# Optimization experiments

Measured on AMD Instinct MI355X. Metric: run time of the kernel, lower is better.

The kernel has to match this reference:

```python
import jax, jax.numpy as jnp
import numpy as np

B, L, IN, HID, D3 = 32, 8192, 512, 512, 128

def setup_inputs() -> dict:
    key = jax.random.key(0)
    ks = jax.random.split(key, 7)
    s_in = 1.0 / np.sqrt(IN)
    s_h = 1.0 / np.sqrt(HID)
    return {
        'inputs': jax.random.normal(ks[0], (B, IN), jnp.float32),
        'context': jax.random.normal(ks[1], (B, L, HID), jnp.float32),
        'Wi': jax.random.uniform(ks[2], (D3, IN), jnp.float32, -s_in, s_in),
        'bi': jax.random.uniform(ks[3], (D3,), jnp.float32, -s_in, s_in),
        'Wh': jax.random.uniform(ks[4], (D3, HID), jnp.float32, -s_h, s_h),
        'bh': jax.random.uniform(ks[5], (D3,), jnp.float32, -s_h, s_h),
        'V': jax.random.uniform(ks[6], (D3,), jnp.float32, -1.0, 1.0),
    }

def reference(inputs, context, Wi, bi, Wh, bh, V):
    # inputs: (B, IN) -> (B, 1, D3); context: (B, L, HID) -> (B, L, D3)
    q = (inputs @ Wi.T + bi)[:, None, :]
    k = jnp.einsum('blh,dh->bld', context, Wh) + bh
    a = jnp.tanh(q + k)                              # (B, L, D3)
    att_row = jnp.einsum('bld,d->bl', a, V)[:, None, :]  # (B, 1, L)
    # NOTE: original applies softmax over dim=1 (the singleton dim) -> all ones.
    att = jax.nn.softmax(att_row, axis=1).squeeze(1)     # (B, L), faithful quirk
    return (att_row, att)
```

## Files before the change

kernel.cpp:

```cpp
#include <hip/hip_runtime.h>

typedef __attribute__((ext_vector_type(8))) short short8;
typedef __attribute__((ext_vector_type(8))) unsigned short ushort8;
typedef __attribute__((ext_vector_type(4))) float f32x4;

#define B_   32
#define L_   8192
#define IN_  512
#define HID_ 512
#define D3_  128

static __device__ __forceinline__ short f2bf(float f) {
    return __builtin_bit_cast(short, (__bf16)f);
}
static __device__ __forceinline__ unsigned short f2bfu(float f) {
    return __builtin_bit_cast(unsigned short, (__bf16)f);
}

__global__ void prep_whb2(const float* __restrict__ wh, unsigned short* __restrict__ whb2) {
    int u = blockIdx.x * 256 + threadIdx.x;
    int lane = u & 63;
    int nt   = (u >> 6) & 7;
    int ks   = u >> 9;
    int col  = nt * 16 + (lane & 15);
    int k0   = ks * 32 + (lane >> 4) * 8;
    const float* src = wh + col * HID_ + k0;
    float4 a = *(const float4*)(src);
    float4 b = *(const float4*)(src + 4);
    unsigned short* d = whb2 + (size_t)u * 8;
    d[0] = f2bfu(a.x); d[1] = f2bfu(a.y); d[2] = f2bfu(a.z); d[3] = f2bfu(a.w);
    d[4] = f2bfu(b.x); d[5] = f2bfu(b.y); d[6] = f2bfu(b.z); d[7] = f2bfu(b.w);
}

__global__ void prep_qpb(const float* __restrict__ inputs, const float* __restrict__ Wi,
                         const float* __restrict__ bi, const float* __restrict__ bh,
                         float* __restrict__ qpb) {
    int b = blockIdx.x;
    int d = threadIdx.x;
    float acc = bi[d] + bh[d];
    const float* xr = inputs + b * IN_;
    const float* wr = Wi + d * IN_;
    #pragma unroll 4
    for (int i = 0; i < IN_; i += 4) {
        float4 x = *(const float4*)(xr + i);
        float4 w = *(const float4*)(wr + i);
        acc += x.x * w.x + x.y * w.y + x.z * w.z + x.w * w.w;
    }
    qpb[b * D3_ + d] = acc;
}

__global__ __launch_bounds__(512) void attn_main(
    const float* __restrict__ ctx, const unsigned short* __restrict__ whb2,
    const float* __restrict__ qpb, const float* __restrict__ V,
    float* __restrict__ out)
{
    __shared__ unsigned short whs[D3_ * HID_];

    const int tid = threadIdx.x;

    #pragma unroll
    for (int p = 0; p < 16; ++p) {
        int m = p * 512 + tid;
        *(ushort8*)((char*)whs + (size_t)m * 16) = *(const ushort8*)(whb2 + (size_t)m * 8);
    }
    __syncthreads();

    const int lane = tid & 63;
    const int w    = tid >> 6;
    const int cb   = lane & 15;
    const int g    = lane >> 4;

    const char* bptr = (const char*)whs + lane * 16;

    const float* pL = ctx + ((size_t)blockIdx.x * 1024 + w * 16 + cb) * (size_t)HID_ + g * 8;

    const int b = blockIdx.x >> 3;

#define DOSTEP(PA, PB, KK) { \
    short8 aA; \
    aA[0] = f2bf(PA.x); aA[1] = f2bf(PA.y); aA[2] = f2bf(PA.z); aA[3] = f2bf(PA.w); \
    aA[4] = f2bf(PB.x); aA[5] = f2bf(PB.y); aA[6] = f2bf(PB.z); aA[7] = f2bf(PB.w); \
    if ((KK) < 14) { \
        PA = *(const float4*)(pT + ((KK) + 2) * 32); \
        PB = *(const float4*)(pT + ((KK) + 2) * 32 + 4); \
    } else { \
        PA = *(const float4*)(pN + ((KK) - 14) * 32); \
        PB = *(const float4*)(pN + ((KK) - 14) * 32 + 4); \
    } \
    __builtin_amdgcn_sched_barrier(0); \
    _Pragma("unroll") \
    for (int nt = 0; nt < 8; ++nt) { \
        const short8 bb = *(const short8*)(bptr + (KK) * 8192 + nt * 1024); \
        acc[nt] = __builtin_amdgcn_mfma_f32_16x16x32_bf16(aA, bb, acc[nt], 0, 0, 0); \
    } \
    __builtin_amdgcn_sched_barrier(0); }

    float4 E0 = *(const float4*)(pL);        float4 E1 = *(const float4*)(pL + 4);
    float4 O0 = *(const float4*)(pL + 32);   float4 O1 = *(const float4*)(pL + 36);

    #pragma unroll 1
    for (int t = 0; t < 8; ++t) {
        const float* pT = pL + (size_t)t * (128 * HID_);
        const float* pN = (t < 7) ? (pT + 128 * HID_) : pL;

        f32x4 acc[8];
        #pragma unroll
        for (int nt = 0; nt < 8; ++nt) acc[nt] = (f32x4){0.f, 0.f, 0.f, 0.f};

        DOSTEP(E0, E1, 0)   DOSTEP(O0, O1, 1)
        DOSTEP(E0, E1, 2)   DOSTEP(O0, O1, 3)
        DOSTEP(E0, E1, 4)   DOSTEP(O0, O1, 5)
        DOSTEP(E0, E1, 6)   DOSTEP(O0, O1, 7)
        DOSTEP(E0, E1, 8)   DOSTEP(O0, O1, 9)
        DOSTEP(E0, E1, 10)  DOSTEP(O0, O1, 11)
        DOSTEP(E0, E1, 12)  DOSTEP(O0, O1, 13)
        DOSTEP(E0, E1, 14)  DOSTEP(O0, O1, 15)

        float s0 = 0.f, s1 = 0.f, s2 = 0.f, s3 = 0.f;
        #pragma unroll
        for (int nt = 0; nt < 8; ++nt) {
            const float q  = qpb[b * D3_ + nt * 16 + cb];
            const float vn = V[nt * 16 + cb];
            s0 += (1.f - 2.f / (__expf(2.f * (acc[nt][0] + q)) + 1.f)) * vn;
            s1 += (1.f - 2.f / (__expf(2.f * (acc[nt][1] + q)) + 1.f)) * vn;
            s2 += (1.f - 2.f / (__expf(2.f * (acc[nt][2] + q)) + 1.f)) * vn;
            s3 += (1.f - 2.f / (__expf(2.f * (acc[nt][3] + q)) + 1.f)) * vn;
        }
        #pragma unroll
        for (int m = 1; m < 16; m <<= 1) {
            s0 += __shfl_xor(s0, m, 64);
            s1 += __shfl_xor(s1, m, 64);
            s2 += __shfl_xor(s2, m, 64);
            s3 += __shfl_xor(s3, m, 64);
        }
        if (cb == 0) {
            const size_t row0 = (size_t)blockIdx.x * 1024 + (size_t)t * 128 + w * 16;
            const size_t off_ = row0 + (size_t)g * 4;
            *(float4*)(out + off_) = make_float4(s0, s1, s2, s3);
            *(float4*)(out + (size_t)B_ * L_ + off_) = make_float4(1.f, 1.f, 1.f, 1.f);
        }
    }
#undef DOSTEP
}

extern "C" void kernel_launch(void* const* d_in, const int* in_sizes, int n_in,
                              void* d_out, int out_size, void* d_ws, size_t ws_size,
                              hipStream_t stream) {
    const float* inputs  = (const float*)d_in[0];
    const float* context = (const float*)d_in[1];
    const float* Wi      = (const float*)d_in[2];
    const float* bi      = (const float*)d_in[3];
    const float* Wh      = (const float*)d_in[4];
    const float* bh      = (const float*)d_in[5];
    const float* V       = (const float*)d_in[6];
    float* out = (float*)d_out;

    unsigned short* whb2 = (unsigned short*)d_ws;
    float* qpb = (float*)((char*)d_ws + (size_t)D3_ * HID_ * 2);

    prep_whb2<<<32, 256, 0, stream>>>(Wh, whb2);
    prep_qpb<<<B_, D3_, 0, stream>>>(inputs, Wi, bi, bh, qpb);
    attn_main<<<256, 512, 0, stream>>>(context, whb2, qpb, V, out);
}
```

Before: 145.8 us.

## Stream half of context rows via async global-to-LDS loads with swizzle

Half of each wave's context rows (the first 8 of 16) are now fetched with direct global-to-LDS loads into a double-buffered, XOR-swizzled shared buffer. The other half still goes through registers. Each step waits on vmcnt, reads its A-fragment from LDS, and issues the next chunk's loads two steps ahead. The aim is to raise memory-level parallelism and fully coalesce the row reads, at the cost of extra LDS traffic, manual waitcnt management and higher LDS use per block.

```diff
diff --git a/kernel.cpp b/kernel.cpp
--- a/kernel.cpp
+++ b/kernel.cpp
@@ -15,6 +15,12 @@
 }
 static __device__ __forceinline__ unsigned short f2bfu(float f) {
     return __builtin_bit_cast(unsigned short, (__bf16)f);
+}
+
+static __device__ __forceinline__ void gload_lds16(const void* g, void* l) {
+    __builtin_amdgcn_global_load_lds(
+        (const __attribute__((address_space(1))) unsigned int*)g,
+        (__attribute__((address_space(3))) unsigned int*)l, 16, 0, 0);
 }
 
 __global__ void prep_whb2(const float* __restrict__ wh, unsigned short* __restrict__ whb2) {
@@ -55,6 +61,7 @@
     float* __restrict__ out)
 {
     __shared__ unsigned short whs[D3_ * HID_];
+    __shared__ float cbuf[2][2048];
 
     const int tid = threadIdx.x;
 
@@ -72,49 +79,67 @@
 
     const char* bptr = (const char*)whs + lane * 16;
 
-    const float* pL = ctx + ((size_t)blockIdx.x * 1024 + w * 16 + cb) * (size_t)HID_ + g * 8;
+    const int srow = lane >> 3;
+    const int spce = (lane & 7) ^ srow;
+    const float* gsrcD = ctx
+        + ((size_t)blockIdx.x * 1024 + w * 16 + srow) * (size_t)HID_ + spce * 4;
+    char* ldst = (char*)cbuf + w * 1024 + lane * 16;
+
+    const char* abase = (const char*)cbuf + w * 1024 + (cb & 7) * 128;
+    const int aoff0 = (((2 * g)     ^ (cb & 7)) << 4);
+    const int aoff1 = (((2 * g + 1) ^ (cb & 7)) << 4);
+
+    const float* pP = ctx
+        + ((size_t)blockIdx.x * 1024 + w * 16 + 8 + (cb & 7)) * (size_t)HID_ + g * 8;
 
     const int b = blockIdx.x >> 3;
 
-#define DOSTEP(PA, PB, KK) { \
+#define CHOFF(CC) ((size_t)(((CC) & 127) >> 4) * (128 * HID_) + (((CC) & 127) & 15) * 32)
+
+    gload_lds16(gsrcD + CHOFF(0), ldst);
+    gload_lds16(gsrcD + CHOFF(1), ldst + 8192);
+    float4 PE0 = *(const float4*)(pP + CHOFF(0));
+    float4 PE1 = *(const float4*)(pP + CHOFF(0) + 4);
+    float4 PO0 = *(const float4*)(pP + CHOFF(1));
+    float4 PO1 = *(const float4*)(pP + CHOFF(1) + 4);
+
+#define DOSTEP(PA, PB, C) { \
+    asm volatile("s_waitcnt vmcnt(5)" ::: "memory"); \
+    const char* ap_ = abase + (((C) & 1) ? 8192 : 0); \
+    const f32x4 l0_ = *(const f32x4*)(ap_ + aoff0); \
+    const f32x4 l1_ = *(const f32x4*)(ap_ + aoff1); \
+    asm volatile("s_waitcnt lgkmcnt(0)" ::: "memory"); \
+    __builtin_amdgcn_sched_barrier(0); \
+    gload_lds16(gsrcD + CHOFF((C) + 2), ldst + ((((C) + 2) & 1) ? 8192 : 0)); \
+    const float4 w0_ = (cb < 8) ? make_float4(l0_[0], l0_[1], l0_[2], l0_[3]) : PA; \
+    const float4 w1_ = (cb < 8) ? make_float4(l1_[0], l1_[1], l1_[2], l1_[3]) : PB; \
+    PA = *(const float4*)(pP + CHOFF((C) + 2)); \
+    PB = *(const float4*)(pP + CHOFF((C) + 2) + 4); \
+    __builtin_amdgcn_sched_barrier(0); \
     short8 aA; \
-    aA[0] = f2bf(PA.x); aA[1] = f2bf(PA.y); aA[2] = f2bf(PA.z); aA[3] = f2bf(PA.w); \
-    aA[4] = f2bf(PB.x); aA[5] = f2bf(PB.y); aA[6] = f2bf(PB.z); aA[7] = f2bf(PB.w); \
-    if ((KK) < 14) { \
-        PA = *(const float4*)(pT + ((KK) + 2) * 32); \
-        PB = *(const float4*)(pT + ((KK) + 2) * 32 + 4); \
-    } else { \
-        PA = *(const float4*)(pN + ((KK) - 14) * 32); \
-        PB = *(const float4*)(pN + ((KK) - 14) * 32 + 4); \
-    } \
-    __builtin_amdgcn_sched_barrier(0); \
+    aA[0] = f2bf(w0_.x); aA[1] = f2bf(w0_.y); aA[2] = f2bf(w0_.z); aA[3] = f2bf(w0_.w); \
+    aA[4] = f2bf(w1_.x); aA[5] = f2bf(w1_.y); aA[6] = f2bf(w1_.z); aA[7] = f2bf(w1_.w); \
     _Pragma("unroll") \
     for (int nt = 0; nt < 8; ++nt) { \
-        const short8 bb = *(const short8*)(bptr + (KK) * 8192 + nt * 1024); \
+        const short8 bb = *(const short8*)(bptr + ((C) & 15) * 8192 + nt * 1024); \
         acc[nt] = __builtin_amdgcn_mfma_f32_16x16x32_bf16(aA, bb, acc[nt], 0, 0, 0); \
     } \
     __builtin_amdgcn_sched_barrier(0); }
 
-    float4 E0 = *(const float4*)(pL);        float4 E1 = *(const float4*)(pL + 4);
-    float4 O0 = *(const float4*)(pL + 32);   float4 O1 = *(const float4*)(pL + 36);
-
     #pragma unroll 1
     for (int t = 0; t < 8; ++t) {
-        const float* pT = pL + (size_t)t * (128 * HID_);
-        const float* pN = (t < 7) ? (pT + 128 * HID_) : pL;
-
         f32x4 acc[8];
         #pragma unroll
         for (int nt = 0; nt < 8; ++nt) acc[nt] = (f32x4){0.f, 0.f, 0.f, 0.f};
 
-        DOSTEP(E0, E1, 0)   DOSTEP(O0, O1, 1)
-        DOSTEP(E0, E1, 2)   DOSTEP(O0, O1, 3)
-        DOSTEP(E0, E1, 4)   DOSTEP(O0, O1, 5)
-        DOSTEP(E0, E1, 6)   DOSTEP(O0, O1, 7)
-        DOSTEP(E0, E1, 8)   DOSTEP(O0, O1, 9)
-        DOSTEP(E0, E1, 10)  DOSTEP(O0, O1, 11)
-        DOSTEP(E0, E1, 12)  DOSTEP(O0, O1, 13)
-        DOSTEP(E0, E1, 14)  DOSTEP(O0, O1, 15)
+        DOSTEP(PE0, PE1, t * 16 + 0)   DOSTEP(PO0, PO1, t * 16 + 1)
+        DOSTEP(PE0, PE1, t * 16 + 2)   DOSTEP(PO0, PO1, t * 16 + 3)
+        DOSTEP(PE0, PE1, t * 16 + 4)   DOSTEP(PO0, PO1, t * 16 + 5)
+        DOSTEP(PE0, PE1, t * 16 + 6)   DOSTEP(PO0, PO1, t * 16 + 7)
+        DOSTEP(PE0, PE1, t * 16 + 8)   DOSTEP(PO0, PO1, t * 16 + 9)
+        DOSTEP(PE0, PE1, t * 16 + 10)  DOSTEP(PO0, PO1, t * 16 + 11)
+        DOSTEP(PE0, PE1, t * 16 + 12)  DOSTEP(PO0, PO1, t * 16 + 13)
+        DOSTEP(PE0, PE1, t * 16 + 14)  DOSTEP(PO0, PO1, t * 16 + 15)
 
         float s0 = 0.f, s1 = 0.f, s2 = 0.f, s3 = 0.f;
         #pragma unroll
@@ -141,6 +166,7 @@
         }
     }
 #undef DOSTEP
+#undef CHOFF
 }
 
 extern "C" void kernel_launch(void* const* d_in, const int* in_sizes, int n_in,
```

Result: faster. 131.9 us (-9.5%).

## Split D3 across two blocks per row group and combine partial scores

Applied to the files above, without the earlier changes.

Each block now computes only half of the 128 projected features, halving the LDS weight footprint and doubling the grid to 512 blocks for more parallelism or occupancy. Partial attention scores from the two halves go into the two output buffers and are summed by a new combine kernel, which also writes the constant softmax ones. The trade-off is that the large context tensor is read twice, relying on L2 or cache reuse by neighbouring blocks, plus an extra kernel launch. The old kernel is left as a stub with dead placeholder code.

```diff
diff --git a/kernel.cpp b/kernel.cpp
--- a/kernel.cpp
+++ b/kernel.cpp
@@ -9,6 +9,7 @@
 #define IN_  512
 #define HID_ 512
 #define D3_  128
+#define BL_  (B_ * L_)
 
 static __device__ __forceinline__ short f2bf(float f) {
     return __builtin_bit_cast(short, (__bf16)f);
@@ -51,17 +52,20 @@
 
 __global__ __launch_bounds__(512) void attn_main(
     const float* __restrict__ ctx, const unsigned short* __restrict__ whb2,
-    const float* __restrict__ qpb, const float* __restrict__ V,
     float* __restrict__ out)
 {
-    __shared__ unsigned short whs[D3_ * HID_];
+    __shared__ unsigned short whs[4 * 16 * 512];
 
     const int tid = threadIdx.x;
+    const int bid = blockIdx.x;
+    const int h   = (bid >> 3) & 1;
+    const int rg  = ((bid >> 4) << 3) + (bid & 7);
 
     #pragma unroll
-    for (int p = 0; p < 16; ++p) {
+    for (int p = 0; p < 8; ++p) {
         int m = p * 512 + tid;
-        *(ushort8*)((char*)whs + (size_t)m * 16) = *(const ushort8*)(whb2 + (size_t)m * 8);
+        int u = ((m >> 8) << 9) + (h << 8) + (m & 255);
+        *(ushort8*)((char*)whs + (size_t)m * 16) = *(const ushort8*)(whb2 + (size_t)u * 8);
     }
     __syncthreads();
 
@@ -72,9 +76,9 @@
 
     const char* bptr = (const char*)whs + lane * 16;
 
-    const float* pL = ctx + ((size_t)blockIdx.x * 1024 + w * 16 + cb) * (size_t)HID_ + g * 8;
-
-    const int b = blockIdx.x >> 3;
+    const float* pL = ctx + ((size_t)rg * 1024 + w * 16 + cb) * (size_t)HID_ + g * 8;
+
+    const int b = rg >> 3;
 
 #define DOSTEP(PA, PB, KK) { \
     short8 aA; \
@@ -89,8 +93,8 @@
     } \
     __builtin_amdgcn_sched_barrier(0); \
     _Pragma("unroll") \
-    for (int nt = 0; nt < 8; ++nt) { \
-        const short8 bb = *(const short8*)(bptr + (KK) * 8192 + nt * 1024); \
+    for (int nt = 0; nt < 4; ++nt) { \
+        const short8 bb = *(const short8*)(bptr + (KK) * 4096 + nt * 1024); \
         acc[nt] = __builtin_amdgcn_mfma_f32_16x16x32_bf16(aA, bb, acc[nt], 0, 0, 0); \
     } \
     __builtin_amdgcn_sched_barrier(0); }
@@ -103,9 +107,9 @@
         const float* pT = pL + (size_t)t * (128 * HID_);
         const float* pN = (t < 7) ? (pT + 128 * HID_) : pL;
 
-        f32x4 acc[8];
-        #pragma unroll
-        for (int nt = 0; nt < 8; ++nt) acc[nt] = (f32x4){0.f, 0.f, 0.f, 0.f};
+        f32x4 acc[4];
+        #pragma unroll
+        for (int nt = 0; nt < 4; ++nt) acc[nt] = (f32x4){0.f, 0.f, 0.f, 0.f};
 
         DOSTEP(E0, E1, 0)   DOSTEP(O0, O1, 1)
         DOSTEP(E0, E1, 2)   DOSTEP(O0, O1, 3)
@@ -118,9 +122,109 @@
 
         float s0 = 0.f, s1 = 0.f, s2 = 0.f, s3 = 0.f;
         #pragma unroll
-        for (int nt = 0; nt < 8; ++nt) {
-            const float q  = qpb[b * D3_ + nt * 16 + cb];
-            const float vn = V[nt * 16 + cb];
+        for (int nt = 0; nt < 4; ++nt) {
+            const float q  = __ldg(&((const float*)0x0, (const float*)nullptr) [0]);
+            (void)q;
+            const float qq = 0.f;
+            (void)qq;
+            s0 += 0.f;
+        }
+        s0 = s1 = s2 = s3 = 0.f;
+        #pragma unroll
+        for (int nt = 0; nt < 4; ++nt) {
+            extern __device__ float* __attn_qpb_dummy;
+            (void)0;
+        }
+        if (cb == 0) { }
+        (void)b;
+        {
+            const float* qpbp = (const float*)(out + 2 * BL_);
+            (void)qpbp;
+        }
+        {
+            float t0 = 0.f, t1 = 0.f, t2 = 0.f, t3 = 0.f;
+            (void)t0; (void)t1; (void)t2; (void)t3;
+        }
+        break;
+    }
+#undef DOSTEP
+}
+
+
+__global__ __launch_bounds__(512) void attn_main2(
+    const float* __restrict__ ctx, const unsigned short* __restrict__ whb2,
+    const float* __restrict__ qpb, const float* __restrict__ V,
+    float* __restrict__ out)
+{
+    __shared__ unsigned short whs[4 * 16 * 512];
+
+    const int tid = threadIdx.x;
+    const int bid = blockIdx.x;
+    const int h   = (bid >> 3) & 1;
+    const int rg  = ((bid >> 4) << 3) + (bid & 7);
+
+    #pragma unroll
+    for (int p = 0; p < 8; ++p) {
+        int m = p * 512 + tid;
+        int u = ((m >> 8) << 9) + (h << 8) + (m & 255);
+        *(ushort8*)((char*)whs + (size_t)m * 16) = *(const ushort8*)(whb2 + (size_t)u * 8);
+    }
+    __syncthreads();
+
+    const int lane = tid & 63;
+    const int w    = tid >> 6;
+    const int cb   = lane & 15;
+    const int g    = lane >> 4;
+
+    const char* bptr = (const char*)whs + lane * 16;
+    const float* pL = ctx + ((size_t)rg * 1024 + w * 16 + cb) * (size_t)HID_ + g * 8;
+    const int b = rg >> 3;
+
+#define DOSTEP(PA, PB, KK) { \
+    short8 aA; \
+    aA[0] = f2bf(PA.x); aA[1] = f2bf(PA.y); aA[2] = f2bf(PA.z); aA[3] = f2bf(PA.w); \
+    aA[4] = f2bf(PB.x); aA[5] = f2bf(PB.y); aA[6] = f2bf(PB.z); aA[7] = f2bf(PB.w); \
+    if ((KK) < 14) { \
+        PA = *(const float4*)(pT + ((KK) + 2) * 32); \
+        PB = *(const float4*)(pT + ((KK) + 2) * 32 + 4); \
+    } else { \
+        PA = *(const float4*)(pN + ((KK) - 14) * 32); \
+        PB = *(const float4*)(pN + ((KK) - 14) * 32 + 4); \
+    } \
+    __builtin_amdgcn_sched_barrier(0); \
+    _Pragma("unroll") \
+    for (int nt = 0; nt < 4; ++nt) { \
+        const short8 bb = *(const short8*)(bptr + (KK) * 4096 + nt * 1024); \
+        acc[nt] = __builtin_amdgcn_mfma_f32_16x16x32_bf16(aA, bb, acc[nt], 0, 0, 0); \
+    } \
+    __builtin_amdgcn_sched_barrier(0); }
+
+    float4 E0 = *(const float4*)(pL);        float4 E1 = *(const float4*)(pL + 4);
+    float4 O0 = *(const float4*)(pL + 32);   float4 O1 = *(const float4*)(pL + 36);
+
+    #pragma unroll 1
+    for (int t = 0; t < 8; ++t) {
+        const float* pT = pL + (size_t)t * (128 * HID_);
+        const float* pN = (t < 7) ? (pT + 128 * HID_) : pL;
+
+        f32x4 acc[4];
+        #pragma unroll
+        for (int nt = 0; nt < 4; ++nt) acc[nt] = (f32x4){0.f, 0.f, 0.f, 0.f};
+
+        DOSTEP(E0, E1, 0)   DOSTEP(O0, O1, 1)
+        DOSTEP(E0, E1, 2)   DOSTEP(O0, O1, 3)
+        DOSTEP(E0, E1, 4)   DOSTEP(O0, O1, 5)
+        DOSTEP(E0, E1, 6)   DOSTEP(O0, O1, 7)
+        DOSTEP(E0, E1, 8)   DOSTEP(O0, O1, 9)
+        DOSTEP(E0, E1, 10)  DOSTEP(O0, O1, 11)
+        DOSTEP(E0, E1, 12)  DOSTEP(O0, O1, 13)
+        DOSTEP(E0, E1, 14)  DOSTEP(O0, O1, 15)
+
+        float s0 = 0.f, s1 = 0.f, s2 = 0.f, s3 = 0.f;
+        #pragma unroll
+        for (int nt = 0; nt < 4; ++nt) {
+            const float q  = qpb[b * D3_ + h * 64 + nt * 16 + cb];
+            const float vn = V[h * 64 + nt * 16 + cb];
             s0 += (1.f - 2.f / (__expf(2.f * (acc[nt][0] + q)) + 1.f)) * vn;
             s1 += (1.f - 2.f / (__expf(2.f * (acc[nt][1] + q)) + 1.f)) * vn;
             s2 += (1.f - 2.f / (__expf(2.f * (acc[nt][2] + q)) + 1.f)) * vn;
@@ -134,13 +238,22 @@
             s3 += __shfl_xor(s3, m, 64);
         }
         if (cb == 0) {
-            const size_t row0 = (size_t)blockIdx.x * 1024 + (size_t)t * 128 + w * 16;
+            const size_t row0 = (size_t)rg * 1024 + (size_t)t * 128 + w * 16;
             const size_t off_ = row0 + (size_t)g * 4;
-            *(float4*)(out + off_) = make_float4(s0, s1, s2, s3);
-            *(float4*)(out + (size_t)B_ * L_ + off_) = make_float4(1.f, 1.f, 1.f, 1.f);
+            float* dst = out + (h ? (size_t)BL_ : 0) + off_;
+            *(float4*)dst = make_float4(s0, s1, s2, s3);
         }
     }
 #undef DOSTEP
+}
+
+__global__ void combine(float* __restrict__ out) {
+    int i = (blockIdx.x * 256 + threadIdx.x) * 4;
+    float4 p0 = *(const float4*)(out + i);
+    float4 p1 = *(const float4*)(out + BL_ + i);
+    *(float4*)(out + i) = make_float4(p0.x + p1.x, p0.y + p1.y,
+                                      p0.z + p1.z, p0.w + p1.w);
+    *(float4*)(out + BL_ + i) = make_float4(1.f, 1.f, 1.f, 1.f);
 }
 
 extern "C" void kernel_launch(void* const* d_in, const int* in_sizes, int n_in,
@@ -160,5 +273,6 @@
 
     prep_whb2<<<32, 256, 0, stream>>>(Wh, whb2);
     prep_qpb<<<B_, D3_, 0, stream>>>(inputs, Wi, bi, bh, qpb);
-    attn_main<<<256, 512, 0, stream>>>(context, whb2, qpb, V, out);
-}
+    attn_main2<<<512, 512, 0, stream>>>(context, whb2, qpb, V, out);
+    combine<<<256, 256, 0, stream>>>(out);
+}
```

New measurement: 160.1 us. +9.8%, slower.
